# Kernel optimization log

Measured on AMD Instinct MI355X. Metric: run time of the kernel, lower is better.

The kernel has to match this reference:

```python
import jax, jax.numpy as jnp
import numpy as np

N = 50000
E = 800000
IN_CH = 256
HEADS = 4
OUT_CH = 32
NEG_SLOPE = 0.2
EPS = 1e-16


def setup_inputs() -> dict:
    key = jax.random.key(0)
    k1, k2, k3, k4 = jax.random.split(key, 4)
    x = jax.random.normal(k1, (N, IN_CH), dtype=jnp.float32)
    edge_index = jax.random.randint(k2, (2, E), 0, N, dtype=jnp.int32)
    # xavier-ish scaling for stability
    weight = jax.random.normal(k3, (HEADS, IN_CH, OUT_CH), dtype=jnp.float32) * (1.0 / np.sqrt(IN_CH))
    att = jax.random.normal(k4, (HEADS, 2 * OUT_CH), dtype=jnp.float32) * (1.0 / np.sqrt(2 * OUT_CH))
    bias = jnp.zeros((HEADS * OUT_CH,), dtype=jnp.float32)
    return {"x": x, "edge_index": edge_index, "weight": weight, "att": att, "bias": bias}


def reference(x, edge_index, weight, att, bias):
    n = x.shape[0]
    H, C = weight.shape[0], weight.shape[2]
    src, dst = edge_index[0], edge_index[1]
    # node features -> per-head projected features [N,H,C]
    h = jnp.einsum('nf,hfc->nhc', x, weight)
    # per-node attention logits (equivalent to concat([h_src,h_dst]) . att)
    a_src = jnp.einsum('nhc,hc->nh', h, att[:, :C])  # [N,H]
    a_dst = jnp.einsum('nhc,hc->nh', h, att[:, C:])  # [N,H]
    alpha = a_src[src] + a_dst[dst]                  # [E,H]
    alpha = jnp.where(alpha > 0, alpha, NEG_SLOPE * alpha)  # LeakyReLU(0.2)
    # segment softmax over incoming edges of each dst node
    alpha_max = jnp.full((n, H), -1e9, dtype=alpha.dtype).at[dst].max(alpha)
    alpha_exp = jnp.exp(alpha - alpha_max[dst])
    sum_exp = jax.ops.segment_sum(alpha_exp, dst, num_segments=n)  # [N,H]
    a = alpha_exp / (sum_exp[dst] + EPS)             # [E,H]
    # weighted scatter-add aggregation
    msg = h[src] * a[:, :, None]                     # [E,H,C]
    out = jax.ops.segment_sum(msg, dst, num_segments=n)  # [N,H,C]
    out = out.reshape(n, H * C) + bias[None, :]
    return out
```

## Files before the change

### kernel.cpp

```cpp
#include <hip/hip_runtime.h>
#include <hip/hip_bf16.h>

#define NEG_SLOPE 0.2f
#define EPSF 1e-16f

typedef __attribute__((ext_vector_type(8))) short short8;
typedef __attribute__((ext_vector_type(4))) float floatx4;

__device__ __forceinline__ float bf2f(unsigned short u) {
  union { unsigned int i; float f; } v; v.i = ((unsigned int)u) << 16; return v.f;
}
__device__ __forceinline__ unsigned short f2bf(float f) {
  union { float f; unsigned int i; } v; v.f = f;
  unsigned int r = v.i + 0x7fffu + ((v.i >> 16) & 1u);
  return (unsigned short)(r >> 16);
}

__global__ __launch_bounds__(256) void prep_k(const unsigned short* __restrict__ xw,
                                              const void* __restrict__ w,
                                              const void* __restrict__ att,
                                              const void* __restrict__ bias,
                                              int* __restrict__ flag,
                                              int* __restrict__ cursor,
                                              int* __restrict__ ovf_cnt,
                                              unsigned short* __restrict__ bpack,
                                              unsigned short* __restrict__ wpack,
                                              float* __restrict__ bias_f,
                                              int n, int zb) {
  int b = blockIdx.x;
  if (b < zb) {
    int i = b * 256 + threadIdx.x;
    if (i < n) cursor[i] = 0;
    if (i == 0) *ovf_cnt = 0;
    return;
  }
  __shared__ int cnt;
  if (threadIdx.x == 0) cnt = 0;
  __syncthreads();
  int local = 0;
  for (int k2 = 0; k2 < 16; k2++) {
    unsigned short u = xw[(threadIdx.x * 16 + k2) << 1];
    int ex = (u >> 7) & 0xFF;
    if (ex >= 0x90 || ex <= 0x40) local++;
  }
  atomicAdd(&cnt, local);
  __syncthreads();
  int f32 = (cnt > 256) ? 1 : 0;
  int pb = b - zb;
  if (pb == 0 && threadIdx.x == 0) *flag = f32;
  if (pb < 128) {
    int i = pb * 256 + threadIdx.x;
    int j = i & 7, lane = (i >> 3) & 63, nt = (i >> 9) & 7, kb = i >> 12;
    int f = (kb << 5) + ((lane >> 4) << 3) + j;
    int col = (nt << 4) + (lane & 15);
    int src = ((col >> 5) << 13) + (f << 5) + (col & 31);
    float v = f32 ? ((const float*)w)[src] : bf2f(((const unsigned short*)w)[src]);
    bpack[i] = f2bf(v);
  } else if (pb < 144) {
    int i = (pb - 128) * 256 + threadIdx.x;
    int j = i & 7, lane = (i >> 3) & 63, kb = i >> 9;
    int quad = lane >> 4, m16 = lane & 15;
    int f = (kb << 5) + (quad << 3) + j;
    float v = 0.f;
    if (m16 < 8) {
      int hd = m16 & 3;
      int db = (m16 >= 4) ? 32 : 0;
      int wbase = (hd << 13) + (f << 5);
      int abase = (hd << 6) + db;
      float acc = 0.f;
      for (int c = 0; c < 32; c++) {
        float wv = f32 ? ((const float*)w)[wbase + c] : bf2f(((const unsigned short*)w)[wbase + c]);
        float av = f32 ? ((const float*)att)[abase + c] : bf2f(((const unsigned short*)att)[abase + c]);
        acc = fmaf(wv, av, acc);
      }
      v = acc;
    }
    wpack[i] = f2bf(v);
  } else {
    int i = threadIdx.x;
    if (i < 128) bias_f[i] = f32 ? ((const float*)bias)[i] : bf2f(((const unsigned short*)bias)[i]);
  }
}

__global__ __launch_bounds__(256) void gemmfill_k(const void* __restrict__ xv,
                                                  const int* __restrict__ flag,
                                                  const unsigned short* __restrict__ bpack,
                                                  const unsigned short* __restrict__ wpack,
                                                  unsigned short* __restrict__ h,
                                                  float* __restrict__ a_srcp,
                                                  float* __restrict__ a_dstp,
                                                  const int* __restrict__ ei,
                                                  int* __restrict__ cursor,
                                                  unsigned short* __restrict__ ed,
                                                  int2* __restrict__ ovf,
                                                  int* __restrict__ ovf_cnt,
                                                  int n, int e, int gb, int fb) {
  int b = blockIdx.x;
  if (b < gb) {
    int t = threadIdx.x;
    int wave = t >> 6, l = t & 63;
    int quad = l >> 4, m16 = l & 15;
    long n0 = (long)b * 128 + wave * 32;
    int isf32 = *flag;

    floatx4 acc[2][8];
    floatx4 acca[2];
#pragma unroll
    for (int mt = 0; mt < 2; mt++) {
      acca[mt] = (floatx4){0.f, 0.f, 0.f, 0.f};
#pragma unroll
      for (int nt = 0; nt < 8; nt++) acc[mt][nt] = (floatx4){0.f, 0.f, 0.f, 0.f};
    }

    for (int kb = 0; kb < 8; kb++) {
      short8 afr[2];
#pragma unroll
      for (int mt = 0; mt < 2; mt++) {
        long row = n0 + mt * 16 + m16;
        if (row >= n) row = n - 1;
        if (isf32) {
          const float* xp = (const float*)xv + (row << 8) + (kb << 5) + (quad << 3);
          float4 u0 = *(const float4*)xp;
          float4 u1 = *(const float4*)(xp + 4);
          short8 a;
          a[0] = (short)f2bf(u0.x); a[1] = (short)f2bf(u0.y);
          a[2] = (short)f2bf(u0.z); a[3] = (short)f2bf(u0.w);
          a[4] = (short)f2bf(u1.x); a[5] = (short)f2bf(u1.y);
          a[6] = (short)f2bf(u1.z); a[7] = (short)f2bf(u1.w);
          afr[mt] = a;
        } else {
          afr[mt] = *(const short8*)((const unsigned short*)xv + (row << 8) + (kb << 5) + (quad << 3));
        }
      }
      short8 wfr = *(const short8*)(wpack + (((kb << 6) + l) << 3));
      acca[0] = __builtin_amdgcn_mfma_f32_16x16x32_bf16(afr[0], wfr, acca[0], 0, 0, 0);
      acca[1] = __builtin_amdgcn_mfma_f32_16x16x32_bf16(afr[1], wfr, acca[1], 0, 0, 0);
#pragma unroll
      for (int nt = 0; nt < 8; nt++) {
        short8 bfr = *(const short8*)(bpack + (((kb << 3) + nt) << 9) + (l << 3));
        acc[0][nt] = __builtin_amdgcn_mfma_f32_16x16x32_bf16(afr[0], bfr, acc[0][nt], 0, 0, 0);
        acc[1][nt] = __builtin_amdgcn_mfma_f32_16x16x32_bf16(afr[1], bfr, acc[1][nt], 0, 0, 0);
      }
    }
#pragma unroll
    for (int mt = 0; mt < 2; mt++)
#pragma unroll
      for (int r = 0; r < 4; r++) {
        long row = n0 + mt * 16 + quad * 4 + r;
        if (row < n) {
#pragma unroll
          for (int nt = 0; nt < 8; nt++)
            h[(row << 7) + (nt << 4) + m16] = f2bf(acc[mt][nt][r]);
          if (m16 < 8) {
            float val = acca[mt][r];
            int hd = m16 & 3;
            if (m16 < 4) a_srcp[(row << 2) + hd] = val;
            else         a_dstp[(row << 2) + hd] = val;
          }
        }
      }
  } else {
    int c = b - gb;
    int i0 = (c << 9) + threadIdx.x;
    int i1 = i0 + 256;
    unsigned d0 = 0, d1 = 0;
    int s0 = 0, s1 = 0;
    bool p0 = (i0 < e), p1 = (i1 < e);
    if (p0) { d0 = (unsigned)ei[e + i0]; s0 = ei[i0]; }
    if (p1) { d1 = (unsigned)ei[e + i1]; s1 = ei[i1]; }
    if (p0 && d0 >= (unsigned)n) p0 = false;
    if (p1 && d1 >= (unsigned)n) p1 = false;
    int c0 = -1, c1 = -1;
    if (p0) { if ((unsigned)s0 >= (unsigned)n) s0 = 0; c0 = atomicAdd(&cursor[d0], 1); }
    if (p1) { if ((unsigned)s1 >= (unsigned)n) s1 = 0; c1 = atomicAdd(&cursor[d1], 1); }
    if (p0) {
      if (c0 < 32) ed[((int)d0 << 5) + c0] = (unsigned short)s0;
      else { int kk = atomicAdd(ovf_cnt, 1); if (kk < e) ovf[kk] = make_int2((int)d0, s0); }
    }
    if (p1) {
      if (c1 < 32) ed[((int)d1 << 5) + c1] = (unsigned short)s1;
      else { int kk = atomicAdd(ovf_cnt, 1); if (kk < e) ovf[kk] = make_int2((int)d1, s1); }
    }
  }
}

__global__ __launch_bounds__(512) void agg_k(const unsigned short* __restrict__ hfeat,
                                             const int* __restrict__ cursor,
                                             const unsigned short* __restrict__ ed,
                                             const int2* __restrict__ ovf,
                                             const int* __restrict__ ovf_cnt,
                                             const float* __restrict__ a_src,
                                             const float* __restrict__ a_dst,
                                             const float* __restrict__ bias_f,
                                             const int* __restrict__ flag,
                                             void* __restrict__ outv, int n, int e) {
  int wave = threadIdx.x >> 6;
  int l = threadIdx.x & 63;
  int node = (blockIdx.x << 3) + wave;
  if (node >= n) return;
  int total = cursor[node];
  int edv = (l < 32) ? (int)ed[(node << 5) + l] : 0;
  float4 ad4 = *(const float4*)&a_dst[node << 2];

  int cnt0 = min(total, 32);
  int hq = l & 3;
  int c8 = l & 15;
  int hg = c8 >> 2;
  int q = l >> 4;
  float adq = (hq == 0) ? ad4.x : (hq == 1) ? ad4.y : (hq == 2) ? ad4.z : ad4.w;

  float m_run = -3.0e38f;
  float swacc = 0.f;
  float acc[8];
#pragma unroll
  for (int k = 0; k < 8; k++) acc[k] = 0.f;

  if (cnt0 > 0) {
    int srcv = (l < cnt0) ? edv : 0;
    int myslot = l >> 2;
    int ssA = __shfl(srcv, myslot, 64);
    int ssB = __shfl(srcv, myslot + 16, 64);
    float asA = (myslot < cnt0) ? a_src[(ssA << 2) + hq] : 0.f;
    float asB = (myslot + 16 < cnt0) ? a_src[(ssB << 2) + hq] : 0.f;
    uint4 hv[8];
    int njs = (cnt0 + 3) >> 2;
#pragma unroll
    for (int j = 0; j < 8; j++) {
      if (j < njs) {
        int sj = __shfl(srcv, (j << 2) + q, 64);
        hv[j] = *(const uint4*)(hfeat + (((size_t)sj) << 7) + (c8 << 3));
      }
    }
    float zA = -3.0e38f, zB = -3.0e38f;
    if (myslot < cnt0) {
      float zz = asA + adq;
      zA = zz > 0.f ? zz : NEG_SLOPE * zz;
    }
    if (myslot + 16 < cnt0) {
      float zz = asB + adq;
      zB = zz > 0.f ? zz : NEG_SLOPE * zz;
    }
    float cm = fmaxf(zA, zB);
    cm = fmaxf(cm, __shfl_xor(cm, 4, 64));
    cm = fmaxf(cm, __shfl_xor(cm, 8, 64));
    cm = fmaxf(cm, __shfl_xor(cm, 16, 64));
    cm = fmaxf(cm, __shfl_xor(cm, 32, 64));
    float wexpA = (myslot < cnt0) ? __expf(zA - cm) : 0.f;
    float wexpB = (myslot + 16 < cnt0) ? __expf(zB - cm) : 0.f;
    m_run = cm;
    swacc = wexpA + wexpB;
#pragma unroll
    for (int j = 0; j < 8; j++) {
      if (j < njs) {
        int eidx = (j << 2) + q;
        float sw = (j < 4) ? __shfl(wexpA, (eidx << 2) | hg, 64)
                           : __shfl(wexpB, ((eidx - 16) << 2) | hg, 64);
        unsigned uu[4] = {hv[j].x, hv[j].y, hv[j].z, hv[j].w};
#pragma unroll
        for (int k2 = 0; k2 < 4; k2++) {
          acc[2 * k2]     = fmaf(sw, bf2f((unsigned short)(uu[k2] & 0xffffu)), acc[2 * k2]);
          acc[2 * k2 + 1] = fmaf(sw, bf2f((unsigned short)(uu[k2] >> 16)), acc[2 * k2 + 1]);
        }
      }
    }
  }

  if (total > 32) {
    int K = *ovf_cnt;
    if (K > e) K = e;
    for (int c0 = 0; c0 < K; c0 += 16) {
      int sv = 0, dv = -1;
      if (l < 16 && (c0 + l) < K) { int2 pr = ovf[c0 + l]; dv = pr.x; sv = pr.y; }
      int myslot = l >> 2;
      int dmy = __shfl(dv, myslot, 64);
      int smy = __shfl(sv, myslot, 64);
      bool valid = (dmy == node);
      float z = -3.0e38f;
      if (valid) {
        float zz = a_src[(smy << 2) + hq] + adq;
        z = zz > 0.f ? zz : NEG_SLOPE * zz;
      }
      float cm = z;
      cm = fmaxf(cm, __shfl_xor(cm, 4, 64));
      cm = fmaxf(cm, __shfl_xor(cm, 8, 64));
      cm = fmaxf(cm, __shfl_xor(cm, 16, 64));
      cm = fmaxf(cm, __shfl_xor(cm, 32, 64));
      float m_new = fmaxf(m_run, cm);
      float resc_q = __expf(m_run - m_new);
      m_run = m_new;
      float wexp = valid ? __expf(z - m_new) : 0.f;
      swacc = swacc * resc_q + wexp;
      float resc_h = __shfl(resc_q, hg, 64);
#pragma unroll
      for (int k = 0; k < 8; k++) acc[k] *= resc_h;
#pragma unroll
      for (int js = 0; js < 4; js++) {
        int eidx = (js << 2) + q;
        float sw = __shfl(wexp, (eidx << 2) | hg, 64);
        int sj = __shfl(sv, eidx, 64);
        uint4 hv = *(const uint4*)(hfeat + (((size_t)sj) << 7) + (c8 << 3));
        unsigned uu[4] = {hv.x, hv.y, hv.z, hv.w};
#pragma unroll
        for (int k2 = 0; k2 < 4; k2++) {
          acc[2 * k2]     = fmaf(sw, bf2f((unsigned short)(uu[k2] & 0xffffu)), acc[2 * k2]);
          acc[2 * k2 + 1] = fmaf(sw, bf2f((unsigned short)(uu[k2] >> 16)), acc[2 * k2 + 1]);
        }
      }
    }
  }

  for (int m = 4; m < 64; m <<= 1) swacc += __shfl_xor(swacc, m, 64);
#pragma unroll
  for (int k = 0; k < 8; k++) {
    acc[k] += __shfl_xor(acc[k], 16, 64);
    acc[k] += __shfl_xor(acc[k], 32, 64);
  }
  float sumv = __shfl(swacc, hg, 64);
  float rs = 1.f / (sumv + EPSF);
  if (l < 16) {
    float o[8];
#pragma unroll
    for (int k = 0; k < 8; k++) o[k] = fmaf(acc[k], rs, bias_f[(c8 << 3) + k]);
    size_t base = (((size_t)node) << 7) + (c8 << 3);
    if (*flag) {
      *(float4*)((float*)outv + base)     = make_float4(o[0], o[1], o[2], o[3]);
      *(float4*)((float*)outv + base + 4) = make_float4(o[4], o[5], o[6], o[7]);
    } else {
      uint4 pk;
      pk.x = (unsigned)f2bf(o[0]) | ((unsigned)f2bf(o[1]) << 16);
      pk.y = (unsigned)f2bf(o[2]) | ((unsigned)f2bf(o[3]) << 16);
      pk.z = (unsigned)f2bf(o[4]) | ((unsigned)f2bf(o[5]) << 16);
      pk.w = (unsigned)f2bf(o[6]) | ((unsigned)f2bf(o[7]) << 16);
      *(uint4*)((unsigned short*)outv + base) = pk;
    }
  }
}

extern "C" void kernel_launch(void* const* d_in, const int* in_sizes, int n_in,
                              void* d_out, int out_size, void* d_ws, size_t ws_size,
                              hipStream_t stream) {
  const void* x    = d_in[0];
  const int*  ei   = (const int*)d_in[1];
  const void* w    = d_in[2];
  const void* att  = d_in[3];
  const void* bias = d_in[4];

  const int n = in_sizes[0] / 256;
  const int e = in_sizes[1] / 2;
  const int zb = (n + 255) / 256;
  const int gb = (n + 127) / 128;
  const int fb = (e + 511) / 512;

  char* p = (char*)d_ws;
  size_t off = 0;
  auto carve = [&](size_t bytes) -> void* {
    void* r = p + off;
    off = (off + bytes + 255) & ~(size_t)255;
    return r;
  };
  int*      flag    = (int*)carve(sizeof(int));
  int*      ovf_cnt = (int*)carve(sizeof(int));
  float*    bias_f  = (float*)carve(128 * 4);
  unsigned short* h = (unsigned short*)carve((size_t)n * 128 * 2);
  float*    a_src   = (float*)carve((size_t)n * 4 * 4);
  float*    a_dst   = (float*)carve((size_t)n * 4 * 4);
  int*      cursor  = (int*)carve((size_t)n * 4);
  unsigned short* ed = (unsigned short*)carve((size_t)n * 32 * 2);
  int2*     ovf     = (int2*)carve((size_t)e * 8);
  unsigned short* bpack = (unsigned short*)carve((size_t)256 * 128 * 2);
  unsigned short* wpack = (unsigned short*)carve((size_t)8 * 64 * 8 * 2);
  (void)ws_size;

  prep_k<<<zb + 145, 256, 0, stream>>>((const unsigned short*)x, w, att, bias,
                                       flag, cursor, ovf_cnt, bpack, wpack, bias_f,
                                       n, zb);
  gemmfill_k<<<gb + fb, 256, 0, stream>>>(x, flag, bpack, wpack, h, a_src, a_dst,
                                          ei, cursor, ed, ovf, ovf_cnt, n, e, gb, fb);
  agg_k<<<(n + 7) / 8, 512, 0, stream>>>(h, cursor, ed, ovf, ovf_cnt, a_src, a_dst,
                                         bias_f, flag, d_out, n, e);
}
```

Measured before the change: 186.9 us.

## Replace per-node atomic edge bucketing with block-local binned counting sort

Edge bucketing now sorts each 4096-edge chunk in shared memory by 128-node destination bin, then reserves space with one global atomic per bin and writes packed (dst,src) pairs into a per-bin arena. The aggregation kernel loads a bin's arena into LDS, counting-sorts it by destination, and then processes nodes of any degree in 32-edge chunks with an online softmax. This is meant to cut the many scattered global atomics and the fixed 32-slot per-node layout with its overflow path. The cost is added LDS passes, barriers and prefix scans in both kernels. The aggregation grid also shrinks to two 512-thread blocks per bin, each wave handling 8 nodes in sequence, which may lower parallelism.

```diff
diff --git a/kernel.cpp b/kernel.cpp
--- a/kernel.cpp
+++ b/kernel.cpp
@@ -3,6 +3,8 @@
 
 #define NEG_SLOPE 0.2f
 #define EPSF 1e-16f
+#define BSH 7
+#define BCAP 4096
 
 typedef __attribute__((ext_vector_type(8))) short short8;
 typedef __attribute__((ext_vector_type(4))) float floatx4;
@@ -21,17 +23,17 @@
                                               const void* __restrict__ att,
                                               const void* __restrict__ bias,
                                               int* __restrict__ flag,
-                                              int* __restrict__ cursor,
-                                              int* __restrict__ ovf_cnt,
+                                              int* __restrict__ bcur,
+                                              int* __restrict__ spill_cnt,
                                               unsigned short* __restrict__ bpack,
                                               unsigned short* __restrict__ wpack,
                                               float* __restrict__ bias_f,
-                                              int n, int zb) {
+                                              int nb, int zb) {
   int b = blockIdx.x;
   if (b < zb) {
     int i = b * 256 + threadIdx.x;
-    if (i < n) cursor[i] = 0;
-    if (i == 0) *ovf_cnt = 0;
+    if (i < nb) bcur[i] = 0;
+    if (i == 0) *spill_cnt = 0;
     return;
   }
   __shared__ int cnt;
@@ -90,10 +92,10 @@
                                                   float* __restrict__ a_srcp,
                                                   float* __restrict__ a_dstp,
                                                   const int* __restrict__ ei,
-                                                  int* __restrict__ cursor,
-                                                  unsigned short* __restrict__ ed,
-                                                  int2* __restrict__ ovf,
-                                                  int* __restrict__ ovf_cnt,
+                                                  int* __restrict__ bcur,
+                                                  unsigned int* __restrict__ arena,
+                                                  int2* __restrict__ spill,
+                                                  int* __restrict__ spill_cnt,
                                                   int n, int e, int gb, int fb) {
   int b = blockIdx.x;
   if (b < gb) {
@@ -160,178 +162,276 @@
         }
       }
   } else {
+    const int NB = (n + 127) >> BSH;
+    __shared__ unsigned int pairL[4096];
+    __shared__ unsigned short loffL[4096];
+    __shared__ unsigned short invL[4096];
+    __shared__ unsigned int lhist[512];
+    __shared__ unsigned int lbase[512];
+    __shared__ unsigned int gbs[512];
+    __shared__ unsigned int stot;
+    int t = threadIdx.x;
     int c = b - gb;
-    int i0 = (c << 9) + threadIdx.x;
-    int i1 = i0 + 256;
-    unsigned d0 = 0, d1 = 0;
-    int s0 = 0, s1 = 0;
-    bool p0 = (i0 < e), p1 = (i1 < e);
-    if (p0) { d0 = (unsigned)ei[e + i0]; s0 = ei[i0]; }
-    if (p1) { d1 = (unsigned)ei[e + i1]; s1 = ei[i1]; }
-    if (p0 && d0 >= (unsigned)n) p0 = false;
-    if (p1 && d1 >= (unsigned)n) p1 = false;
-    int c0 = -1, c1 = -1;
-    if (p0) { if ((unsigned)s0 >= (unsigned)n) s0 = 0; c0 = atomicAdd(&cursor[d0], 1); }
-    if (p1) { if ((unsigned)s1 >= (unsigned)n) s1 = 0; c1 = atomicAdd(&cursor[d1], 1); }
-    if (p0) {
-      if (c0 < 32) ed[((int)d0 << 5) + c0] = (unsigned short)s0;
-      else { int kk = atomicAdd(ovf_cnt, 1); if (kk < e) ovf[kk] = make_int2((int)d0, s0); }
-    }
-    if (p1) {
-      if (c1 < 32) ed[((int)d1 << 5) + c1] = (unsigned short)s1;
-      else { int kk = atomicAdd(ovf_cnt, 1); if (kk < e) ovf[kk] = make_int2((int)d1, s1); }
+    for (int i = t; i < NB; i += 256) lhist[i] = 0;
+    __syncthreads();
+    int e0 = c << 12;
+#pragma unroll
+    for (int j = 0; j < 16; j++) {
+      int idx = (j << 8) + t;
+      int i = e0 + idx;
+      unsigned pv = 0xFFFF0000u;
+      if (i < e) {
+        unsigned d = (unsigned)ei[e + i];
+        if (d < (unsigned)n) {
+          unsigned s = (unsigned)ei[i];
+          if (s >= (unsigned)n) s = 0;
+          pv = (d << 16) | s;
+          unsigned lo = atomicAdd(&lhist[d >> BSH], 1u);
+          loffL[idx] = (unsigned short)lo;
+        }
+      }
+      pairL[idx] = pv;
+    }
+    __syncthreads();
+    unsigned a0 = (2 * t < NB) ? lhist[2 * t] : 0u;
+    unsigned a1 = (2 * t + 1 < NB) ? lhist[2 * t + 1] : 0u;
+    gbs[t] = a0 + a1;
+    __syncthreads();
+    for (int off = 1; off < 256; off <<= 1) {
+      unsigned v = (t >= off) ? gbs[t - off] : 0u;
+      __syncthreads();
+      gbs[t] += v;
+      __syncthreads();
+    }
+    unsigned excl = gbs[t] - (a0 + a1);
+    if (t == 255) stot = gbs[255];
+    if (2 * t < NB) lbase[2 * t] = excl;
+    if (2 * t + 1 < NB) lbase[2 * t + 1] = excl + a0;
+    __syncthreads();
+    for (int kk = t; kk < NB; kk += 256) {
+      unsigned cc = lhist[kk];
+      gbs[kk] = cc ? (unsigned)atomicAdd(&bcur[kk], (int)cc) : 0u;
+    }
+#pragma unroll
+    for (int j = 0; j < 16; j++) {
+      int idx = (j << 8) + t;
+      unsigned pv = pairL[idx];
+      if ((pv >> 16) < (unsigned)n)
+        invL[lbase[(pv >> 16) >> BSH] + loffL[idx]] = (unsigned short)idx;
+    }
+    __syncthreads();
+    unsigned tot = stot;
+    for (unsigned sp = t; sp < tot; sp += 256) {
+      int idx = (int)invL[sp];
+      unsigned pv = pairL[idx];
+      unsigned k = pv >> (16 + BSH);
+      unsigned pos = gbs[k] + (sp - lbase[k]);
+      if (pos < (unsigned)BCAP) {
+        arena[(k << 12) + pos] = pv;
+      } else {
+        int s2 = atomicAdd(spill_cnt, 1);
+        if (s2 < e) spill[s2] = make_int2((int)(pv >> 16), (int)(pv & 0xFFFFu));
+      }
     }
   }
 }
 
 __global__ __launch_bounds__(512) void agg_k(const unsigned short* __restrict__ hfeat,
-                                             const int* __restrict__ cursor,
-                                             const unsigned short* __restrict__ ed,
-                                             const int2* __restrict__ ovf,
-                                             const int* __restrict__ ovf_cnt,
+                                             const int* __restrict__ bcur,
+                                             const unsigned int* __restrict__ arena,
+                                             const int2* __restrict__ spill,
+                                             const int* __restrict__ spill_cnt,
                                              const float* __restrict__ a_src,
                                              const float* __restrict__ a_dst,
                                              const float* __restrict__ bias_f,
                                              const int* __restrict__ flag,
                                              void* __restrict__ outv, int n, int e) {
-  int wave = threadIdx.x >> 6;
-  int l = threadIdx.x & 63;
-  int node = (blockIdx.x << 3) + wave;
-  if (node >= n) return;
-  int total = cursor[node];
-  int edv = (l < 32) ? (int)ed[(node << 5) + l] : 0;
-  float4 ad4 = *(const float4*)&a_dst[node << 2];
-
-  int cnt0 = min(total, 32);
+  const int NB = (n + 127) >> BSH;
+  int bk = (int)(blockIdx.x >> 1);
+  int half = (int)(blockIdx.x & 1);
+  if (bk >= NB) return;
+  __shared__ unsigned int parr[BCAP];
+  __shared__ unsigned short srcs[BCAP];
+  __shared__ unsigned int degL[128], offL[128], curL[128];
+  int t = threadIdx.x;
+  unsigned total_claim = (unsigned)bcur[bk];
+  int cnt = (int)((total_claim < (unsigned)BCAP) ? total_claim : (unsigned)BCAP);
+  bool spilled = total_claim > (unsigned)BCAP;
+  if (t < 128) degL[t] = 0;
+  __syncthreads();
+  for (int i = t; i < cnt; i += 512) {
+    unsigned pv = arena[((unsigned)bk << 12) + i];
+    parr[i] = pv;
+    atomicAdd(&degL[(pv >> 16) & 127], 1u);
+  }
+  __syncthreads();
+  if (t < 128) offL[t] = degL[t];
+  __syncthreads();
+  for (int off = 1; off < 128; off <<= 1) {
+    unsigned v = 0;
+    if (t < 128 && t >= off) v = offL[t - off];
+    __syncthreads();
+    if (t < 128) offL[t] += v;
+    __syncthreads();
+  }
+  if (t < 128) { unsigned ex = offL[t] - degL[t]; offL[t] = ex; curL[t] = ex; }
+  __syncthreads();
+  for (int i = t; i < cnt; i += 512) {
+    unsigned pv = parr[i];
+    unsigned lo = atomicAdd(&curL[(pv >> 16) & 127], 1u);
+    srcs[lo] = (unsigned short)(pv & 0xFFFFu);
+  }
+  __syncthreads();
+
+  int wave = t >> 6;
+  int l = t & 63;
   int hq = l & 3;
   int c8 = l & 15;
   int hg = c8 >> 2;
   int q = l >> 4;
-  float adq = (hq == 0) ? ad4.x : (hq == 1) ? ad4.y : (hq == 2) ? ad4.z : ad4.w;
-
-  float m_run = -3.0e38f;
-  float swacc = 0.f;
-  float acc[8];
-#pragma unroll
-  for (int k = 0; k < 8; k++) acc[k] = 0.f;
-
-  if (cnt0 > 0) {
-    int srcv = (l < cnt0) ? edv : 0;
-    int myslot = l >> 2;
-    int ssA = __shfl(srcv, myslot, 64);
-    int ssB = __shfl(srcv, myslot + 16, 64);
-    float asA = (myslot < cnt0) ? a_src[(ssA << 2) + hq] : 0.f;
-    float asB = (myslot + 16 < cnt0) ? a_src[(ssB << 2) + hq] : 0.f;
-    uint4 hv[8];
-    int njs = (cnt0 + 3) >> 2;
-#pragma unroll
-    for (int j = 0; j < 8; j++) {
-      if (j < njs) {
-        int sj = __shfl(srcv, (j << 2) + q, 64);
-        hv[j] = *(const uint4*)(hfeat + (((size_t)sj) << 7) + (c8 << 3));
-      }
-    }
-    float zA = -3.0e38f, zB = -3.0e38f;
-    if (myslot < cnt0) {
-      float zz = asA + adq;
-      zA = zz > 0.f ? zz : NEG_SLOPE * zz;
-    }
-    if (myslot + 16 < cnt0) {
-      float zz = asB + adq;
-      zB = zz > 0.f ? zz : NEG_SLOPE * zz;
-    }
-    float cm = fmaxf(zA, zB);
-    cm = fmaxf(cm, __shfl_xor(cm, 4, 64));
-    cm = fmaxf(cm, __shfl_xor(cm, 8, 64));
-    cm = fmaxf(cm, __shfl_xor(cm, 16, 64));
-    cm = fmaxf(cm, __shfl_xor(cm, 32, 64));
-    float wexpA = (myslot < cnt0) ? __expf(zA - cm) : 0.f;
-    float wexpB = (myslot + 16 < cnt0) ? __expf(zB - cm) : 0.f;
-    m_run = cm;
-    swacc = wexpA + wexpB;
-#pragma unroll
-    for (int j = 0; j < 8; j++) {
-      if (j < njs) {
-        int eidx = (j << 2) + q;
-        float sw = (j < 4) ? __shfl(wexpA, (eidx << 2) | hg, 64)
-                           : __shfl(wexpB, ((eidx - 16) << 2) | hg, 64);
-        unsigned uu[4] = {hv[j].x, hv[j].y, hv[j].z, hv[j].w};
-#pragma unroll
-        for (int k2 = 0; k2 < 4; k2++) {
-          acc[2 * k2]     = fmaf(sw, bf2f((unsigned short)(uu[k2] & 0xffffu)), acc[2 * k2]);
-          acc[2 * k2 + 1] = fmaf(sw, bf2f((unsigned short)(uu[k2] >> 16)), acc[2 * k2 + 1]);
-        }
-      }
-    }
-  }
-
-  if (total > 32) {
-    int K = *ovf_cnt;
-    if (K > e) K = e;
-    for (int c0 = 0; c0 < K; c0 += 16) {
-      int sv = 0, dv = -1;
-      if (l < 16 && (c0 + l) < K) { int2 pr = ovf[c0 + l]; dv = pr.x; sv = pr.y; }
-      int myslot = l >> 2;
-      int dmy = __shfl(dv, myslot, 64);
-      int smy = __shfl(sv, myslot, 64);
-      bool valid = (dmy == node);
-      float z = -3.0e38f;
-      if (valid) {
-        float zz = a_src[(smy << 2) + hq] + adq;
-        z = zz > 0.f ? zz : NEG_SLOPE * zz;
-      }
-      float cm = z;
+  int myslot = l >> 2;
+  int isf32 = *flag;
+
+  for (int jj = 0; jj < 8; jj++) {
+    int d7 = (half << 6) + (wave << 3) + jj;
+    int node = (bk << BSH) + d7;
+    if (node >= n) continue;
+    int deg = (int)degL[d7];
+    int noff = (int)offL[d7];
+    float4 ad4 = *(const float4*)&a_dst[node << 2];
+    float adq = (hq == 0) ? ad4.x : (hq == 1) ? ad4.y : (hq == 2) ? ad4.z : ad4.w;
+
+    float m_run = -3.0e38f;
+    float swacc = 0.f;
+    float acc[8];
+#pragma unroll
+    for (int k = 0; k < 8; k++) acc[k] = 0.f;
+
+    for (int base = 0; base < deg; base += 32) {
+      int cntb = min(deg - base, 32);
+      int srcv = 0;
+      if (l < cntb) srcv = (int)srcs[noff + base + l];
+      int ssA = __shfl(srcv, myslot, 64);
+      int ssB = __shfl(srcv, myslot + 16, 64);
+      float zA = -3.0e38f, zB = -3.0e38f;
+      if (myslot < cntb) {
+        float zz = a_src[(ssA << 2) + hq] + adq;
+        zA = zz > 0.f ? zz : NEG_SLOPE * zz;
+      }
+      if (myslot + 16 < cntb) {
+        float zz = a_src[(ssB << 2) + hq] + adq;
+        zB = zz > 0.f ? zz : NEG_SLOPE * zz;
+      }
+      float cm = fmaxf(zA, zB);
       cm = fmaxf(cm, __shfl_xor(cm, 4, 64));
       cm = fmaxf(cm, __shfl_xor(cm, 8, 64));
       cm = fmaxf(cm, __shfl_xor(cm, 16, 64));
       cm = fmaxf(cm, __shfl_xor(cm, 32, 64));
       float m_new = fmaxf(m_run, cm);
-      float resc_q = __expf(m_run - m_new);
+      float resc = __expf(m_run - m_new);
+      float wexpA = (myslot < cntb) ? __expf(zA - m_new) : 0.f;
+      float wexpB = (myslot + 16 < cntb) ? __expf(zB - m_new) : 0.f;
+      swacc = swacc * resc + wexpA + wexpB;
+      float resc_h = __shfl(resc, hg, 64);
+#pragma unroll
+      for (int k = 0; k < 8; k++) acc[k] *= resc_h;
       m_run = m_new;
-      float wexp = valid ? __expf(z - m_new) : 0.f;
-      swacc = swacc * resc_q + wexp;
-      float resc_h = __shfl(resc_q, hg, 64);
-#pragma unroll
-      for (int k = 0; k < 8; k++) acc[k] *= resc_h;
-#pragma unroll
-      for (int js = 0; js < 4; js++) {
-        int eidx = (js << 2) + q;
-        float sw = __shfl(wexp, (eidx << 2) | hg, 64);
-        int sj = __shfl(sv, eidx, 64);
-        uint4 hv = *(const uint4*)(hfeat + (((size_t)sj) << 7) + (c8 << 3));
-        unsigned uu[4] = {hv.x, hv.y, hv.z, hv.w};
-#pragma unroll
-        for (int k2 = 0; k2 < 4; k2++) {
-          acc[2 * k2]     = fmaf(sw, bf2f((unsigned short)(uu[k2] & 0xffffu)), acc[2 * k2]);
-          acc[2 * k2 + 1] = fmaf(sw, bf2f((unsigned short)(uu[k2] >> 16)), acc[2 * k2 + 1]);
-        }
-      }
-    }
-  }
-
-  for (int m = 4; m < 64; m <<= 1) swacc += __shfl_xor(swacc, m, 64);
-#pragma unroll
-  for (int k = 0; k < 8; k++) {
-    acc[k] += __shfl_xor(acc[k], 16, 64);
-    acc[k] += __shfl_xor(acc[k], 32, 64);
-  }
-  float sumv = __shfl(swacc, hg, 64);
-  float rs = 1.f / (sumv + EPSF);
-  if (l < 16) {
-    float o[8];
-#pragma unroll
-    for (int k = 0; k < 8; k++) o[k] = fmaf(acc[k], rs, bias_f[(c8 << 3) + k]);
-    size_t base = (((size_t)node) << 7) + (c8 << 3);
-    if (*flag) {
-      *(float4*)((float*)outv + base)     = make_float4(o[0], o[1], o[2], o[3]);
-      *(float4*)((float*)outv + base + 4) = make_float4(o[4], o[5], o[6], o[7]);
-    } else {
-      uint4 pk;
-      pk.x = (unsigned)f2bf(o[0]) | ((unsigned)f2bf(o[1]) << 16);
-      pk.y = (unsigned)f2bf(o[2]) | ((unsigned)f2bf(o[3]) << 16);
-      pk.z = (unsigned)f2bf(o[4]) | ((unsigned)f2bf(o[5]) << 16);
-      pk.w = (unsigned)f2bf(o[6]) | ((unsigned)f2bf(o[7]) << 16);
-      *(uint4*)((unsigned short*)outv + base) = pk;
+      uint4 hv[8];
+      int njs = (cntb + 3) >> 2;
+#pragma unroll
+      for (int j = 0; j < 8; j++) {
+        if (j < njs) {
+          int sj = __shfl(srcv, (j << 2) + q, 64);
+          hv[j] = *(const uint4*)(hfeat + (((size_t)sj) << 7) + (c8 << 3));
+        }
+      }
+#pragma unroll
+      for (int j = 0; j < 8; j++) {
+        if (j < njs) {
+          int eidx = (j << 2) + q;
+          float sw = (j < 4) ? __shfl(wexpA, (eidx << 2) | hg, 64)
+                             : __shfl(wexpB, ((eidx - 16) << 2) | hg, 64);
+          unsigned uu[4] = {hv[j].x, hv[j].y, hv[j].z, hv[j].w};
+#pragma unroll
+          for (int k2 = 0; k2 < 4; k2++) {
+            acc[2 * k2]     = fmaf(sw, bf2f((unsigned short)(uu[k2] & 0xffffu)), acc[2 * k2]);
+            acc[2 * k2 + 1] = fmaf(sw, bf2f((unsigned short)(uu[k2] >> 16)), acc[2 * k2 + 1]);
+          }
+        }
+      }
+    }
+
+    if (spilled) {
+      int K = *spill_cnt;
+      if (K > e) K = e;
+      for (int c0 = 0; c0 < K; c0 += 16) {
+        int sv = 0, dv = -1;
+        if (l < 16 && (c0 + l) < K) { int2 pr = spill[c0 + l]; dv = pr.x; sv = pr.y; }
+        int dmy = __shfl(dv, myslot, 64);
+        int smy = __shfl(sv, myslot, 64);
+        bool valid = (dmy == node);
+        float z = -3.0e38f;
+        if (valid) {
+          float zz = a_src[(smy << 2) + hq] + adq;
+          z = zz > 0.f ? zz : NEG_SLOPE * zz;
+        }
+        float cm = z;
+        cm = fmaxf(cm, __shfl_xor(cm, 4, 64));
+        cm = fmaxf(cm, __shfl_xor(cm, 8, 64));
+        cm = fmaxf(cm, __shfl_xor(cm, 16, 64));
+        cm = fmaxf(cm, __shfl_xor(cm, 32, 64));
+        float m_new = fmaxf(m_run, cm);
+        float resc_q = __expf(m_run - m_new);
+        m_run = m_new;
+        float wexp = valid ? __expf(z - m_new) : 0.f;
+        swacc = swacc * resc_q + wexp;
+        float resc_h = __shfl(resc_q, hg, 64);
+#pragma unroll
+        for (int k = 0; k < 8; k++) acc[k] *= resc_h;
+#pragma unroll
+        for (int js = 0; js < 4; js++) {
+          int eidx = (js << 2) + q;
+          float sw = __shfl(wexp, (eidx << 2) | hg, 64);
+          int sj = __shfl(sv, eidx, 64);
+          uint4 hv = *(const uint4*)(hfeat + (((size_t)sj) << 7) + (c8 << 3));
+          unsigned uu[4] = {hv.x, hv.y, hv.z, hv.w};
+#pragma unroll
+          for (int k2 = 0; k2 < 4; k2++) {
+            acc[2 * k2]     = fmaf(sw, bf2f((unsigned short)(uu[k2] & 0xffffu)), acc[2 * k2]);
+            acc[2 * k2 + 1] = fmaf(sw, bf2f((unsigned short)(uu[k2] >> 16)), acc[2 * k2 + 1]);
+          }
+        }
+      }
+    }
+
+    float sw2 = swacc;
+    for (int m = 4; m < 64; m <<= 1) sw2 += __shfl_xor(sw2, m, 64);
+    float ac2[8];
+#pragma unroll
+    for (int k = 0; k < 8; k++) {
+      float a = acc[k];
+      a += __shfl_xor(a, 16, 64);
+      a += __shfl_xor(a, 32, 64);
+      ac2[k] = a;
+    }
+    float sumv = __shfl(sw2, hg, 64);
+    float rs = 1.f / (sumv + EPSF);
+    if (l < 16) {
+      float o[8];
+#pragma unroll
+      for (int k = 0; k < 8; k++) o[k] = fmaf(ac2[k], rs, bias_f[(c8 << 3) + k]);
+      size_t base = (((size_t)node) << 7) + (c8 << 3);
+      if (isf32) {
+        *(float4*)((float*)outv + base)     = make_float4(o[0], o[1], o[2], o[3]);
+        *(float4*)((float*)outv + base + 4) = make_float4(o[4], o[5], o[6], o[7]);
+      } else {
+        uint4 pk;
+        pk.x = (unsigned)f2bf(o[0]) | ((unsigned)f2bf(o[1]) << 16);
+        pk.y = (unsigned)f2bf(o[2]) | ((unsigned)f2bf(o[3]) << 16);
+        pk.z = (unsigned)f2bf(o[4]) | ((unsigned)f2bf(o[5]) << 16);
+        pk.w = (unsigned)f2bf(o[6]) | ((unsigned)f2bf(o[7]) << 16);
+        *(uint4*)((unsigned short*)outv + base) = pk;
+      }
     }
   }
 }
@@ -347,9 +447,10 @@
 
   const int n = in_sizes[0] / 256;
   const int e = in_sizes[1] / 2;
-  const int zb = (n + 255) / 256;
+  const int NB = (n + 127) / 128;
+  const int zb = (NB + 255) / 256;
   const int gb = (n + 127) / 128;
-  const int fb = (e + 511) / 512;
+  const int fb = (e + 4095) / 4096;
 
   char* p = (char*)d_ws;
   size_t off = 0;
@@ -358,24 +459,24 @@
     off = (off + bytes + 255) & ~(size_t)255;
     return r;
   };
-  int*      flag    = (int*)carve(sizeof(int));
-  int*      ovf_cnt = (int*)carve(sizeof(int));
-  float*    bias_f  = (float*)carve(128 * 4);
-  unsigned short* h = (unsigned short*)carve((size_t)n * 128 * 2);
-  float*    a_src   = (float*)carve((size_t)n * 4 * 4);
-  float*    a_dst   = (float*)carve((size_t)n * 4 * 4);
-  int*      cursor  = (int*)carve((size_t)n * 4);
-  unsigned short* ed = (unsigned short*)carve((size_t)n * 32 * 2);
-  int2*     ovf     = (int2*)carve((size_t)e * 8);
+  int*      flag      = (int*)carve(sizeof(int));
+  int*      spill_cnt = (int*)carve(sizeof(int));
+  float*    bias_f    = (float*)carve(128 * 4);
+  unsigned short* h   = (unsigned short*)carve((size_t)n * 128 * 2);
+  float*    a_src     = (float*)carve((size_t)n * 4 * 4);
+  float*    a_dst     = (float*)carve((size_t)n * 4 * 4);
+  int*      bcur      = (int*)carve((size_t)NB * 4);
+  unsigned int* arena = (unsigned int*)carve((size_t)NB * BCAP * 4);
+  int2*     spill     = (int2*)carve((size_t)e * 8);
   unsigned short* bpack = (unsigned short*)carve((size_t)256 * 128 * 2);
   unsigned short* wpack = (unsigned short*)carve((size_t)8 * 64 * 8 * 2);
   (void)ws_size;
 
   prep_k<<<zb + 145, 256, 0, stream>>>((const unsigned short*)x, w, att, bias,
-                                       flag, cursor, ovf_cnt, bpack, wpack, bias_f,
-                                       n, zb);
+                                       flag, bcur, spill_cnt, bpack, wpack, bias_f,
+                                       NB, zb);
   gemmfill_k<<<gb + fb, 256, 0, stream>>>(x, flag, bpack, wpack, h, a_src, a_dst,
-                                          ei, cursor, ed, ovf, ovf_cnt, n, e, gb, fb);
-  agg_k<<<(n + 7) / 8, 512, 0, stream>>>(h, cursor, ed, ovf, ovf_cnt, a_src, a_dst,
-                                         bias_f, flag, d_out, n, e);
-}
+                                          ei, bcur, arena, spill, spill_cnt, n, e, gb, fb);
+  agg_k<<<NB * 2, 512, 0, stream>>>(h, bcur, arena, spill, spill_cnt, a_src, a_dst,
+                                    bias_f, flag, d_out, n, e);
+}
```

Result: slower. 247.1 us (+32.2%).

## Bucket edges by destination block before building per-node adjacency lists

Applied to the files above, without the earlier changes.

Replaces the per-edge global atomic on a per-node cursor with a two-level bucket sort. Edges are first binned into 128-node buckets using shared-memory histograms plus one global atomic per bucket per block. A new kernel then scatters each bucket into per-node slot lists in LDS and writes them out with coalesced stores. The aim is to cut scattered global atomics and random 2-byte writes, at the cost of an extra kernel launch, an intermediate arena buffer and a spill flag packed into the cursor.

```diff
diff --git a/kernel.cpp b/kernel.cpp
--- a/kernel.cpp
+++ b/kernel.cpp
@@ -3,6 +3,8 @@
 
 #define NEG_SLOPE 0.2f
 #define EPSF 1e-16f
+#define BSH 7
+#define BCAP 4096
 
 typedef __attribute__((ext_vector_type(8))) short short8;
 typedef __attribute__((ext_vector_type(4))) float floatx4;
@@ -21,16 +23,16 @@
                                               const void* __restrict__ att,
                                               const void* __restrict__ bias,
                                               int* __restrict__ flag,
-                                              int* __restrict__ cursor,
+                                              int* __restrict__ bcur,
                                               int* __restrict__ ovf_cnt,
                                               unsigned short* __restrict__ bpack,
                                               unsigned short* __restrict__ wpack,
                                               float* __restrict__ bias_f,
-                                              int n, int zb) {
+                                              int nb, int zb) {
   int b = blockIdx.x;
   if (b < zb) {
     int i = b * 256 + threadIdx.x;
-    if (i < n) cursor[i] = 0;
+    if (i < nb) bcur[i] = 0;
     if (i == 0) *ovf_cnt = 0;
     return;
   }
@@ -90,8 +92,8 @@
                                                   float* __restrict__ a_srcp,
                                                   float* __restrict__ a_dstp,
                                                   const int* __restrict__ ei,
-                                                  int* __restrict__ cursor,
-                                                  unsigned short* __restrict__ ed,
+                                                  int* __restrict__ bcur,
+                                                  unsigned int* __restrict__ arena,
                                                   int2* __restrict__ ovf,
                                                   int* __restrict__ ovf_cnt,
                                                   int n, int e, int gb, int fb) {
@@ -160,28 +162,83 @@
         }
       }
   } else {
+    const int NB = (n + 127) >> BSH;
+    __shared__ unsigned int lhist[512];
+    __shared__ unsigned int gbase[512];
+    int t = threadIdx.x;
     int c = b - gb;
-    int i0 = (c << 9) + threadIdx.x;
-    int i1 = i0 + 256;
-    unsigned d0 = 0, d1 = 0;
-    int s0 = 0, s1 = 0;
-    bool p0 = (i0 < e), p1 = (i1 < e);
-    if (p0) { d0 = (unsigned)ei[e + i0]; s0 = ei[i0]; }
-    if (p1) { d1 = (unsigned)ei[e + i1]; s1 = ei[i1]; }
-    if (p0 && d0 >= (unsigned)n) p0 = false;
-    if (p1 && d1 >= (unsigned)n) p1 = false;
-    int c0 = -1, c1 = -1;
-    if (p0) { if ((unsigned)s0 >= (unsigned)n) s0 = 0; c0 = atomicAdd(&cursor[d0], 1); }
-    if (p1) { if ((unsigned)s1 >= (unsigned)n) s1 = 0; c1 = atomicAdd(&cursor[d1], 1); }
-    if (p0) {
-      if (c0 < 32) ed[((int)d0 << 5) + c0] = (unsigned short)s0;
-      else { int kk = atomicAdd(ovf_cnt, 1); if (kk < e) ovf[kk] = make_int2((int)d0, s0); }
-    }
-    if (p1) {
-      if (c1 < 32) ed[((int)d1 << 5) + c1] = (unsigned short)s1;
-      else { int kk = atomicAdd(ovf_cnt, 1); if (kk < e) ovf[kk] = make_int2((int)d1, s1); }
-    }
-  }
+    for (int i = t; i < NB; i += 256) lhist[i] = 0;
+    __syncthreads();
+    int e0 = c << 12;
+    unsigned pv[16];
+    int lo[16];
+#pragma unroll
+    for (int j = 0; j < 16; j++) {
+      int i = e0 + (j << 8) + t;
+      pv[j] = 0xFFFF0000u;
+      lo[j] = 0;
+      if (i < e) {
+        unsigned d = (unsigned)ei[e + i];
+        if (d < (unsigned)n) {
+          unsigned s = (unsigned)ei[i];
+          if (s >= (unsigned)n) s = 0;
+          pv[j] = (d << 16) | s;
+          lo[j] = (int)atomicAdd(&lhist[d >> BSH], 1u);
+        }
+      }
+    }
+    __syncthreads();
+    for (int kk = t; kk < NB; kk += 256) {
+      unsigned cc = lhist[kk];
+      gbase[kk] = cc ? (unsigned)atomicAdd(&bcur[kk], (int)cc) : 0u;
+    }
+    __syncthreads();
+#pragma unroll
+    for (int j = 0; j < 16; j++) {
+      unsigned d = pv[j] >> 16;
+      if (d < (unsigned)n) {
+        unsigned bkt = d >> BSH;
+        unsigned pos = gbase[bkt] + (unsigned)lo[j];
+        if (pos < (unsigned)BCAP) arena[(bkt << 12) + pos] = pv[j];
+        else { int kk2 = atomicAdd(ovf_cnt, 1); if (kk2 < e) ovf[kk2] = make_int2((int)d, (int)(pv[j] & 0xFFFFu)); }
+      }
+    }
+  }
+}
+
+__global__ __launch_bounds__(256) void sortb_k(const unsigned int* __restrict__ arena,
+                                               const int* __restrict__ bcur,
+                                               int* __restrict__ cursor,
+                                               unsigned short* __restrict__ ed,
+                                               int2* __restrict__ ovf,
+                                               int* __restrict__ ovf_cnt,
+                                               int n, int e) {
+  int bk = blockIdx.x;
+  __shared__ unsigned short edL[128][32];
+  __shared__ unsigned int deg[128];
+  int t = threadIdx.x;
+  int total = bcur[bk];
+  int cnt = min(total, BCAP);
+  bool spilled = total > BCAP;
+  if (t < 128) deg[t] = 0;
+  __syncthreads();
+  int node0 = bk << BSH;
+  for (int i = t; i < cnt; i += 256) {
+    unsigned pv = arena[((unsigned)bk << 12) + i];
+    int d7 = (int)((pv >> 16) & 127);
+    unsigned s = pv & 0xFFFFu;
+    unsigned slot = atomicAdd(&deg[d7], 1u);
+    if (slot < 32) edL[d7][slot] = (unsigned short)s;
+    else { int kk = atomicAdd(ovf_cnt, 1); if (kk < e) ovf[kk] = make_int2(node0 + d7, (int)s); }
+  }
+  __syncthreads();
+  int lim = n - node0; if (lim > 128) lim = 128;
+  if (lim <= 0) return;
+  const uint4* edv = (const uint4*)&edL[0][0];
+  for (int j = t; j < (lim << 2); j += 256)
+    *(uint4*)(ed + ((size_t)node0 << 5) + ((size_t)j << 3)) = edv[j];
+  if (t < lim)
+    cursor[node0 + t] = (int)deg[t] + (spilled ? (1 << 20) : 0);
 }
 
 __global__ __launch_bounds__(512) void agg_k(const unsigned short* __restrict__ hfeat,
@@ -202,7 +259,8 @@
   int edv = (l < 32) ? (int)ed[(node << 5) + l] : 0;
   float4 ad4 = *(const float4*)&a_dst[node << 2];
 
-  int cnt0 = min(total, 32);
+  int sdeg = total & 0xFFFFF;
+  int cnt0 = min(sdeg, 32);
   int hq = l & 3;
   int c8 = l & 15;
   int hg = c8 >> 2;
@@ -347,9 +405,10 @@
 
   const int n = in_sizes[0] / 256;
   const int e = in_sizes[1] / 2;
-  const int zb = (n + 255) / 256;
+  const int NB = (n + 127) / 128;
+  const int zb = (NB + 255) / 256;
   const int gb = (n + 127) / 128;
-  const int fb = (e + 511) / 512;
+  const int fb = (e + 4095) / 4096;
 
   char* p = (char*)d_ws;
   size_t off = 0;
@@ -364,6 +423,8 @@
   unsigned short* h = (unsigned short*)carve((size_t)n * 128 * 2);
   float*    a_src   = (float*)carve((size_t)n * 4 * 4);
   float*    a_dst   = (float*)carve((size_t)n * 4 * 4);
+  int*      bcur    = (int*)carve((size_t)NB * 4);
+  unsigned int* arena = (unsigned int*)carve((size_t)NB * BCAP * 4);
   int*      cursor  = (int*)carve((size_t)n * 4);
   unsigned short* ed = (unsigned short*)carve((size_t)n * 32 * 2);
   int2*     ovf     = (int2*)carve((size_t)e * 8);
@@ -372,10 +433,11 @@
   (void)ws_size;
 
   prep_k<<<zb + 145, 256, 0, stream>>>((const unsigned short*)x, w, att, bias,
-                                       flag, cursor, ovf_cnt, bpack, wpack, bias_f,
-                                       n, zb);
+                                       flag, bcur, ovf_cnt, bpack, wpack, bias_f,
+                                       NB, zb);
   gemmfill_k<<<gb + fb, 256, 0, stream>>>(x, flag, bpack, wpack, h, a_src, a_dst,
-                                          ei, cursor, ed, ovf, ovf_cnt, n, e, gb, fb);
+                                          ei, bcur, arena, ovf, ovf_cnt, n, e, gb, fb);
+  sortb_k<<<NB, 256, 0, stream>>>(arena, bcur, cursor, ed, ovf, ovf_cnt, n, e);
   agg_k<<<(n + 7) / 8, 512, 0, stream>>>(h, cursor, ed, ovf, ovf_cnt, a_src, a_dst,
                                          bias_f, flag, d_out, n, e);
 }
```

Measured after the change: 171.6 us. 1.09x faster.
